# Kernel tuning notes

Hardware: AMD Instinct MI355X
Metric: run time of the kernel (lower is better)

Reference implementation:

```python
import jax, jax.numpy as jnp
import numpy as np

H = 1024
V = 50257
S = 4096

def setup_inputs() -> dict:
    key = jax.random.key(0)
    ks = jax.random.split(key, 11)
    inp = {
        "word_input": jax.random.randint(ks[0], (1,), 0, V),
        "last_context": jax.random.normal(ks[1], (1, H), jnp.float32),
        "last_hidden": jax.random.normal(ks[2], (1, 1, H), jnp.float32),
        "encoder_outputs": jax.random.normal(ks[3], (S, 1, H), jnp.float32),
        # parameters
        "embedding": jax.random.normal(ks[4], (V, H), jnp.float32) * 0.02,
        "w_ih": jax.random.normal(ks[5], (3 * H, 2 * H), jnp.float32) * 0.02,
        "w_hh": jax.random.normal(ks[6], (3 * H, H), jnp.float32) * 0.02,
        "b_ih": jax.random.normal(ks[7], (3 * H,), jnp.float32) * 0.02,
        "b_hh": jax.random.normal(ks[8], (3 * H,), jnp.float32) * 0.02,
        "out_w": jax.random.normal(ks[9], (V, 2 * H), jnp.float32) * 0.02,
        "out_b": jax.random.normal(ks[10], (V,), jnp.float32) * 0.02,
    }
    return inp

def reference(word_input, last_context, last_hidden, encoder_outputs,
              embedding, w_ih, w_hh, b_ih, b_hh, out_w, out_b):
    # embedding lookup: [H]
    emb = embedding[word_input[0]]
    # rnn input: cat(embedded, last_context) -> [2H]
    x = jnp.concatenate([emb, last_context[0]])
    h = last_hidden[0, 0]  # [H]
    # PyTorch GRU cell math (gates ordered r, z, n)
    gi = w_ih @ x + b_ih   # [3H]
    gh = w_hh @ h + b_hh   # [3H]
    i_r, i_z, i_n = jnp.split(gi, 3)
    h_r, h_z, h_n = jnp.split(gh, 3)
    r = jax.nn.sigmoid(i_r + h_r)
    z = jax.nn.sigmoid(i_z + h_z)
    n = jnp.tanh(i_n + r * h_n)
    h_new = (1.0 - z) * n + z * h  # [H], == rnn_output.squeeze()
    # multiplicative attention: per-step torch.mm loop == one batched matvec
    enc = encoder_outputs[:, 0, :]          # [S, H]
    scores = enc @ h_new                    # [S]
    attn = jax.nn.softmax(scores)           # softmax over seq dim
    context = attn @ enc                    # [H]
    logits = out_w @ jnp.concatenate([h_new, context]) + out_b  # [V]
    output = jax.nn.log_softmax(logits)[None, :]                # [1, V]
    return (output, context[None, :], h_new[None, None, :], attn[None, None, :])
```

## Files before the change

### kernel.cpp

```cpp
#include <hip/hip_runtime.h>
#include <hip/hip_bf16.h>
#include <math.h>

#define H 1024
#define V 50257
#define S 4096

typedef __hip_bfloat16 bf16;
typedef __attribute__((ext_vector_type(8))) unsigned short ushort8v;
typedef __attribute__((ext_vector_type(4))) unsigned short ushort4v;

#define WS_HX      0
#define WS_CTX     1024
#define WS_SCORES  2048
#define WS_SUMEXP  6144
#define WS_FLAG    6145

#define OUT_LOGSM  0
#define OUT_CTX    V
#define OUT_H      (V + H)
#define OUT_ATTN   (V + 2 * H)

__device__ __forceinline__ float bf2f(unsigned short u) {
    union { unsigned int i; float f; } c;
    c.i = ((unsigned int)u) << 16;
    return c.f;
}

__device__ __forceinline__ float ld1(const void* base, bool isbf, size_t i) {
    return isbf ? bf2f(((const unsigned short*)base)[i]) : ((const float*)base)[i];
}

__device__ __forceinline__ void st1(void* out, bool isbf, size_t i, float v) {
    if (isbf) ((bf16*)out)[i] = __float2bfloat16(v);
    else      ((float*)out)[i] = v;
}

__device__ __forceinline__ float dotrow(const void* base, size_t off, const float* x,
                                        int n, bool isbf, int lane) {
    float acc = 0.f;
    if (isbf) {
        const unsigned short* r = (const unsigned short*)base + off;
        for (int k = lane * 8; k < n; k += 512) {
            ushort8v w = *(const ushort8v*)(r + k);
            float4 a = *(const float4*)(x + k);
            float4 b = *(const float4*)(x + k + 4);
            acc += bf2f(w[0]) * a.x + bf2f(w[1]) * a.y + bf2f(w[2]) * a.z + bf2f(w[3]) * a.w
                 + bf2f(w[4]) * b.x + bf2f(w[5]) * b.y + bf2f(w[6]) * b.z + bf2f(w[7]) * b.w;
        }
    } else {
        const float* r = (const float*)base + off;
        for (int k = lane * 8; k < n; k += 512) {
            float4 wa = *(const float4*)(r + k);
            float4 wb = *(const float4*)(r + k + 4);
            float4 a  = *(const float4*)(x + k);
            float4 b  = *(const float4*)(x + k + 4);
            acc += wa.x * a.x + wa.y * a.y + wa.z * a.z + wa.w * a.w
                 + wb.x * b.x + wb.y * b.y + wb.z * b.z + wb.w * b.w;
        }
    }
    return acc;
}

__global__ __launch_bounds__(64) void k_detect(const unsigned short* __restrict__ lcu,
                                               float* __restrict__ ws)
{
    const int lane = threadIdx.x;
    float x = bf2f(lcu[2 * lane]);
    float ax = fabsf(x);
    int ok = (ax >= 9.5367431640625e-07f && ax <= 64.0f) ? 1 : 0;
    for (int off = 32; off; off >>= 1) ok += __shfl_down(ok, off);
    if (lane == 0) ws[WS_FLAG] = (ok >= 40) ? 1.0f : 0.0f;
}

__global__ __launch_bounds__(256) void k_gru(
    const int* __restrict__ word, const void* __restrict__ lc,
    const void* __restrict__ lh, const void* __restrict__ emb,
    const void* __restrict__ w_ih, const void* __restrict__ w_hh,
    const void* __restrict__ b_ih, const void* __restrict__ b_hh,
    float* __restrict__ ws, void* __restrict__ out)
{
    __shared__ __align__(16) float x[2 * H];
    __shared__ __align__(16) float hb[H];
    const int tid = threadIdx.x;
    const bool isbf = ws[WS_FLAG] > 0.5f;
    const size_t w0 = (size_t)word[0];
    for (int i = tid; i < H; i += 256) {
        x[i]     = ld1(emb, isbf, w0 * H + i);
        x[H + i] = ld1(lc, isbf, i);
        hb[i]    = ld1(lh, isbf, i);
    }
    __syncthreads();

    const int lane = tid & 63, wid = tid >> 6;
    const int i = blockIdx.x * 4 + wid;

    float acc[6];
    for (int g = 0; g < 3; ++g) {
        acc[g]     = dotrow(w_ih, (size_t)(i + g * H) * (2 * H), x,  2 * H, isbf, lane);
        acc[3 + g] = dotrow(w_hh, (size_t)(i + g * H) * H,       hb, H,     isbf, lane);
    }
    for (int off = 32; off; off >>= 1)
        for (int g = 0; g < 6; ++g) acc[g] += __shfl_down(acc[g], off);

    if (lane == 0) {
        float gi_r = acc[0] + ld1(b_ih, isbf, i);
        float gi_z = acc[1] + ld1(b_ih, isbf, i + H);
        float gi_n = acc[2] + ld1(b_ih, isbf, i + 2 * H);
        float gh_r = acc[3] + ld1(b_hh, isbf, i);
        float gh_z = acc[4] + ld1(b_hh, isbf, i + H);
        float gh_n = acc[5] + ld1(b_hh, isbf, i + 2 * H);
        float r = 1.f / (1.f + expf(-(gi_r + gh_r)));
        float z = 1.f / (1.f + expf(-(gi_z + gh_z)));
        float n = tanhf(gi_n + r * gh_n);
        float hn = (1.f - z) * n + z * hb[i];
        ws[WS_HX + i] = hn;
        st1(out, isbf, OUT_H + i, hn);
    }
}

__global__ __launch_bounds__(256) void k_scores(const void* __restrict__ enc,
                                                float* __restrict__ ws)
{
    __shared__ __align__(16) float hx[H];
    const int tid = threadIdx.x;
    const bool isbf = ws[WS_FLAG] > 0.5f;
    for (int i = tid; i < H; i += 256) hx[i] = ws[WS_HX + i];
    __syncthreads();
    const int lane = tid & 63, wid = tid >> 6;
    const int s = blockIdx.x * 4 + wid;
    float acc = dotrow(enc, (size_t)s * H, hx, H, isbf, lane);
    for (int off = 32; off; off >>= 1) acc += __shfl_down(acc, off);
    if (lane == 0) ws[WS_SCORES + s] = acc;
}

__global__ __launch_bounds__(1024) void k_softmax(float* __restrict__ ws, void* __restrict__ out)
{
    const int tid = threadIdx.x, lane = tid & 63, wid = tid >> 6;
    const bool isbf = ws[WS_FLAG] > 0.5f;
    __shared__ float wred[16];
    float v[4];
    float mx = -1e30f;
    for (int q = 0; q < 4; ++q) {
        v[q] = ws[WS_SCORES + tid + q * 1024];
        mx = fmaxf(mx, v[q]);
    }
    for (int off = 32; off; off >>= 1) mx = fmaxf(mx, __shfl_down(mx, off));
    if (lane == 0) wred[wid] = mx;
    __syncthreads();
    if (tid == 0) {
        float m = wred[0];
        for (int i = 1; i < 16; ++i) m = fmaxf(m, wred[i]);
        wred[0] = m;
    }
    __syncthreads();
    const float m = wred[0];
    __syncthreads();
    float se = 0.f;
    for (int q = 0; q < 4; ++q) { v[q] = expf(v[q] - m); se += v[q]; }
    for (int off = 32; off; off >>= 1) se += __shfl_down(se, off);
    if (lane == 0) wred[wid] = se;
    __syncthreads();
    if (tid == 0) {
        float s2 = 0.f;
        for (int i = 0; i < 16; ++i) s2 += wred[i];
        wred[0] = s2;
    }
    __syncthreads();
    const float inv = 1.f / wred[0];
    for (int q = 0; q < 4; ++q) {
        float p = v[q] * inv;
        ws[WS_SCORES + tid + q * 1024] = p;
        st1(out, isbf, OUT_ATTN + tid + q * 1024, p);
    }
    ws[WS_CTX + tid] = 0.f;
    if (tid == 0) ws[WS_SUMEXP] = 0.f;
}

__global__ __launch_bounds__(256) void k_context(const void* __restrict__ enc,
                                                 float* __restrict__ ws)
{
    const int tid = threadIdx.x;
    const bool isbf = ws[WS_FLAG] > 0.5f;
    const int s0 = blockIdx.x * 64;
    const int c0 = 4 * tid;
    float a0 = 0.f, a1 = 0.f, a2 = 0.f, a3 = 0.f;
    if (isbf) {
        const unsigned short* e = (const unsigned short*)enc;
        for (int s = s0; s < s0 + 64; ++s) {
            const float p = ws[WS_SCORES + s];
            ushort4v u = *(const ushort4v*)(e + (size_t)s * H + c0);
            a0 += p * bf2f(u[0]); a1 += p * bf2f(u[1]);
            a2 += p * bf2f(u[2]); a3 += p * bf2f(u[3]);
        }
    } else {
        const float* e = (const float*)enc;
        for (int s = s0; s < s0 + 64; ++s) {
            const float p = ws[WS_SCORES + s];
            float4 u = *(const float4*)(e + (size_t)s * H + c0);
            a0 += p * u.x; a1 += p * u.y; a2 += p * u.z; a3 += p * u.w;
        }
    }
    atomicAdd(&ws[WS_CTX + c0],     a0);
    atomicAdd(&ws[WS_CTX + c0 + 1], a1);
    atomicAdd(&ws[WS_CTX + c0 + 2], a2);
    atomicAdd(&ws[WS_CTX + c0 + 3], a3);
}

__global__ __launch_bounds__(256) void k_logits(
    const void* __restrict__ out_w, const void* __restrict__ out_b,
    float* __restrict__ ws, void* __restrict__ out)
{
    __shared__ __align__(16) float xv[2 * H];
    __shared__ float esum[4];
    const int tid = threadIdx.x;
    const bool isbf = ws[WS_FLAG] > 0.5f;
    for (int i = tid; i < 2 * H; i += 256) xv[i] = ws[WS_HX + i];
    __syncthreads();

    const int lane = tid & 63, wid = tid >> 6;
    const int v = blockIdx.x * 4 + wid;
    float acc = 0.f;
    if (v < V) acc = dotrow(out_w, (size_t)v * (2 * H), xv, 2 * H, isbf, lane);
    for (int off = 32; off; off >>= 1) acc += __shfl_down(acc, off);
    if (lane == 0) {
        float e = 0.f;
        if (v < V) {
            float lg = acc + ld1(out_b, isbf, v);
            st1(out, isbf, OUT_LOGSM + v, lg);
            e = expf(lg);
        }
        esum[wid] = e;
    }
    __syncthreads();
    if (tid == 0) atomicAdd(&ws[WS_SUMEXP], esum[0] + esum[1] + esum[2] + esum[3]);
}

__global__ __launch_bounds__(256) void k_final(float* __restrict__ ws, void* __restrict__ out)
{
    const int idx = blockIdx.x * 256 + threadIdx.x;
    const bool isbf = ws[WS_FLAG] > 0.5f;
    const float logZ = logf(ws[WS_SUMEXP]);
    if (idx < V) {
        float lg = isbf ? bf2f(((const unsigned short*)out)[OUT_LOGSM + idx])
                        : ((const float*)out)[OUT_LOGSM + idx];
        st1(out, isbf, OUT_LOGSM + idx, lg - logZ);
    } else if (idx < V + H) {
        st1(out, isbf, OUT_CTX + (idx - V), ws[WS_CTX + (idx - V)]);
    }
}

extern "C" void kernel_launch(void* const* d_in, const int* in_sizes, int n_in,
                              void* d_out, int out_size, void* d_ws, size_t ws_size,
                              hipStream_t stream) {
    const int* word  = (const int*)d_in[0];
    const void* lc   = d_in[1];
    const void* lh   = d_in[2];
    const void* enc  = d_in[3];
    const void* emb  = d_in[4];
    const void* w_ih = d_in[5];
    const void* w_hh = d_in[6];
    const void* b_ih = d_in[7];
    const void* b_hh = d_in[8];
    const void* o_w  = d_in[9];
    const void* o_b  = d_in[10];
    float* ws = (float*)d_ws;

    k_detect<<<1, 64, 0, stream>>>((const unsigned short*)lc, ws);
    k_gru<<<H / 4, 256, 0, stream>>>(word, lc, lh, emb, w_ih, w_hh, b_ih, b_hh, ws, d_out);
    k_scores<<<S / 4, 256, 0, stream>>>(enc, ws);
    k_softmax<<<1, 1024, 0, stream>>>(ws, d_out);
    k_context<<<S / 64, 256, 0, stream>>>(enc, ws);
    k_logits<<<(V + 3) / 4, 256, 0, stream>>>(o_w, o_b, ws, d_out);
    k_final<<<(V + H + 255) / 256, 256, 0, stream>>>(ws, d_out);
}
```

Measured before the change: 758.5 us.

## Inline dtype detection, restructure GRU per-block rows, use nontemporal weight loads

Removes the separate detection kernel by having each kernel compute the bf16/fp32 flag with a wave ballot on last_context. The GRU kernel now assigns one hidden unit per block, with all 256 threads splitting each row and keeping inputs in registers instead of shared memory. Weight streams for the GRU and logits matrices use nontemporal loads to avoid polluting the cache. The context kernel uses more blocks with 16 rows each, which adds atomics in exchange for more parallelism.

```diff
diff --git a/kernel.cpp b/kernel.cpp
--- a/kernel.cpp
+++ b/kernel.cpp
@@ -9,12 +9,12 @@
 typedef __hip_bfloat16 bf16;
 typedef __attribute__((ext_vector_type(8))) unsigned short ushort8v;
 typedef __attribute__((ext_vector_type(4))) unsigned short ushort4v;
+typedef __attribute__((ext_vector_type(4))) float f32x4;
 
 #define WS_HX      0
 #define WS_CTX     1024
 #define WS_SCORES  2048
 #define WS_SUMEXP  6144
-#define WS_FLAG    6145
 
 #define OUT_LOGSM  0
 #define OUT_CTX    V
@@ -36,13 +36,38 @@
     else      ((float*)out)[i] = v;
 }
 
+__device__ __forceinline__ bool detect_bf(const void* lc) {
+    const unsigned short* lcu = (const unsigned short*)lc;
+    float x = bf2f(lcu[2 * (threadIdx.x & 63)]);
+    float ax = fabsf(x);
+    bool ok = (ax >= 9.5367431640625e-07f && ax <= 64.0f);
+    return __popcll(__ballot(ok)) >= 40;
+}
+
+template<bool NT>
+__device__ __forceinline__ f32x4 ldf4(const float* p) {
+    if (NT) return __builtin_nontemporal_load((const f32x4*)p);
+    return *(const f32x4*)p;
+}
+template<bool NT>
+__device__ __forceinline__ ushort8v ldu8(const unsigned short* p) {
+    if (NT) return __builtin_nontemporal_load((const ushort8v*)p);
+    return *(const ushort8v*)p;
+}
+template<bool NT>
+__device__ __forceinline__ ushort4v ldu4(const unsigned short* p) {
+    if (NT) return __builtin_nontemporal_load((const ushort4v*)p);
+    return *(const ushort4v*)p;
+}
+
+template<bool NT>
 __device__ __forceinline__ float dotrow(const void* base, size_t off, const float* x,
                                         int n, bool isbf, int lane) {
     float acc = 0.f;
     if (isbf) {
         const unsigned short* r = (const unsigned short*)base + off;
         for (int k = lane * 8; k < n; k += 512) {
-            ushort8v w = *(const ushort8v*)(r + k);
+            ushort8v w = ldu8<NT>(r + k);
             float4 a = *(const float4*)(x + k);
             float4 b = *(const float4*)(x + k + 4);
             acc += bf2f(w[0]) * a.x + bf2f(w[1]) * a.y + bf2f(w[2]) * a.z + bf2f(w[3]) * a.w
@@ -51,8 +76,8 @@
     } else {
         const float* r = (const float*)base + off;
         for (int k = lane * 8; k < n; k += 512) {
-            float4 wa = *(const float4*)(r + k);
-            float4 wb = *(const float4*)(r + k + 4);
+            f32x4 wa = ldf4<NT>(r + k);
+            f32x4 wb = ldf4<NT>(r + k + 4);
             float4 a  = *(const float4*)(x + k);
             float4 b  = *(const float4*)(x + k + 4);
             acc += wa.x * a.x + wa.y * a.y + wa.z * a.z + wa.w * a.w
@@ -62,15 +87,29 @@
     return acc;
 }
 
-__global__ __launch_bounds__(64) void k_detect(const unsigned short* __restrict__ lcu,
-                                               float* __restrict__ ws)
-{
-    const int lane = threadIdx.x;
-    float x = bf2f(lcu[2 * lane]);
-    float ax = fabsf(x);
-    int ok = (ax >= 9.5367431640625e-07f && ax <= 64.0f) ? 1 : 0;
-    for (int off = 32; off; off >>= 1) ok += __shfl_down(ok, off);
-    if (lane == 0) ws[WS_FLAG] = (ok >= 40) ? 1.0f : 0.0f;
+template<bool NT>
+__device__ __forceinline__ float dot8row(const void* base, size_t off, const float* xs, bool isbf) {
+    if (isbf) {
+        ushort8v w = ldu8<NT>((const unsigned short*)base + off);
+        return bf2f(w[0]) * xs[0] + bf2f(w[1]) * xs[1] + bf2f(w[2]) * xs[2] + bf2f(w[3]) * xs[3]
+             + bf2f(w[4]) * xs[4] + bf2f(w[5]) * xs[5] + bf2f(w[6]) * xs[6] + bf2f(w[7]) * xs[7];
+    } else {
+        const float* r = (const float*)base + off;
+        f32x4 a = ldf4<NT>(r), b = ldf4<NT>(r + 4);
+        return a.x * xs[0] + a.y * xs[1] + a.z * xs[2] + a.w * xs[3]
+             + b.x * xs[4] + b.y * xs[5] + b.z * xs[6] + b.w * xs[7];
+    }
+}
+
+template<bool NT>
+__device__ __forceinline__ float dot4row(const void* base, size_t off, const float* hs, bool isbf) {
+    if (isbf) {
+        ushort4v w = ldu4<NT>((const unsigned short*)base + off);
+        return bf2f(w[0]) * hs[0] + bf2f(w[1]) * hs[1] + bf2f(w[2]) * hs[2] + bf2f(w[3]) * hs[3];
+    } else {
+        f32x4 a = ldf4<NT>((const float*)base + off);
+        return a.x * hs[0] + a.y * hs[1] + a.z * hs[2] + a.w * hs[3];
+    }
 }
 
 __global__ __launch_bounds__(256) void k_gru(
@@ -80,64 +119,101 @@
     const void* __restrict__ b_ih, const void* __restrict__ b_hh,
     float* __restrict__ ws, void* __restrict__ out)
 {
-    __shared__ __align__(16) float x[2 * H];
-    __shared__ __align__(16) float hb[H];
+    const bool isbf = detect_bf(lc);
     const int tid = threadIdx.x;
-    const bool isbf = ws[WS_FLAG] > 0.5f;
+    const int i = blockIdx.x;
     const size_t w0 = (size_t)word[0];
-    for (int i = tid; i < H; i += 256) {
-        x[i]     = ld1(emb, isbf, w0 * H + i);
-        x[H + i] = ld1(lc, isbf, i);
-        hb[i]    = ld1(lh, isbf, i);
-    }
-    __syncthreads();
-
+
+    float xs[8];
+    {
+        const int k = tid * 8;
+        const void* src = (k < H) ? emb : lc;
+        const size_t o  = (k < H) ? (w0 * H + (size_t)k) : (size_t)(k - H);
+        if (isbf) {
+            ushort8v u = *(const ushort8v*)((const unsigned short*)src + o);
+            #pragma unroll
+            for (int j = 0; j < 8; ++j) xs[j] = bf2f(u[j]);
+        } else {
+            const float* p = (const float*)src + o;
+            f32x4 a = *(const f32x4*)p, b = *(const f32x4*)(p + 4);
+            xs[0] = a.x; xs[1] = a.y; xs[2] = a.z; xs[3] = a.w;
+            xs[4] = b.x; xs[5] = b.y; xs[6] = b.z; xs[7] = b.w;
+        }
+    }
+    float hs[4];
+    {
+        const int k = tid * 4;
+        if (isbf) {
+            ushort4v u = *(const ushort4v*)((const unsigned short*)lh + k);
+            #pragma unroll
+            for (int j = 0; j < 4; ++j) hs[j] = bf2f(u[j]);
+        } else {
+            f32x4 a = *(const f32x4*)((const float*)lh + k);
+            hs[0] = a.x; hs[1] = a.y; hs[2] = a.z; hs[3] = a.w;
+        }
+    }
+
+    float acc[6];
+    #pragma unroll
+    for (int g = 0; g < 3; ++g) {
+        acc[g]     = dot8row<true>(w_ih, (size_t)(i + g * H) * (2 * H) + tid * 8, xs, isbf);
+        acc[3 + g] = dot4row<true>(w_hh, (size_t)(i + g * H) * H + tid * 4, hs, isbf);
+    }
+    #pragma unroll
+    for (int off = 32; off; off >>= 1) {
+        #pragma unroll
+        for (int g = 0; g < 6; ++g) acc[g] += __shfl_down(acc[g], off);
+    }
+
+    __shared__ float wred[4][6];
     const int lane = tid & 63, wid = tid >> 6;
-    const int i = blockIdx.x * 4 + wid;
-
-    float acc[6];
-    for (int g = 0; g < 3; ++g) {
-        acc[g]     = dotrow(w_ih, (size_t)(i + g * H) * (2 * H), x,  2 * H, isbf, lane);
-        acc[3 + g] = dotrow(w_hh, (size_t)(i + g * H) * H,       hb, H,     isbf, lane);
-    }
-    for (int off = 32; off; off >>= 1)
-        for (int g = 0; g < 6; ++g) acc[g] += __shfl_down(acc[g], off);
-
     if (lane == 0) {
-        float gi_r = acc[0] + ld1(b_ih, isbf, i);
-        float gi_z = acc[1] + ld1(b_ih, isbf, i + H);
-        float gi_n = acc[2] + ld1(b_ih, isbf, i + 2 * H);
-        float gh_r = acc[3] + ld1(b_hh, isbf, i);
-        float gh_z = acc[4] + ld1(b_hh, isbf, i + H);
-        float gh_n = acc[5] + ld1(b_hh, isbf, i + 2 * H);
+        #pragma unroll
+        for (int g = 0; g < 6; ++g) wred[wid][g] = acc[g];
+    }
+    __syncthreads();
+    if (tid == 0) {
+        float s[6];
+        #pragma unroll
+        for (int g = 0; g < 6; ++g)
+            s[g] = wred[0][g] + wred[1][g] + wred[2][g] + wred[3][g];
+        float gi_r = s[0] + ld1(b_ih, isbf, i);
+        float gi_z = s[1] + ld1(b_ih, isbf, i + H);
+        float gi_n = s[2] + ld1(b_ih, isbf, i + 2 * H);
+        float gh_r = s[3] + ld1(b_hh, isbf, i);
+        float gh_z = s[4] + ld1(b_hh, isbf, i + H);
+        float gh_n = s[5] + ld1(b_hh, isbf, i + 2 * H);
         float r = 1.f / (1.f + expf(-(gi_r + gh_r)));
         float z = 1.f / (1.f + expf(-(gi_z + gh_z)));
         float n = tanhf(gi_n + r * gh_n);
-        float hn = (1.f - z) * n + z * hb[i];
+        float hbv = ld1(lh, isbf, i);
+        float hn = (1.f - z) * n + z * hbv;
         ws[WS_HX + i] = hn;
         st1(out, isbf, OUT_H + i, hn);
     }
 }
 
 __global__ __launch_bounds__(256) void k_scores(const void* __restrict__ enc,
+                                                const void* __restrict__ lc,
                                                 float* __restrict__ ws)
 {
     __shared__ __align__(16) float hx[H];
+    const bool isbf = detect_bf(lc);
     const int tid = threadIdx.x;
-    const bool isbf = ws[WS_FLAG] > 0.5f;
     for (int i = tid; i < H; i += 256) hx[i] = ws[WS_HX + i];
     __syncthreads();
     const int lane = tid & 63, wid = tid >> 6;
     const int s = blockIdx.x * 4 + wid;
-    float acc = dotrow(enc, (size_t)s * H, hx, H, isbf, lane);
+    float acc = dotrow<false>(enc, (size_t)s * H, hx, H, isbf, lane);
     for (int off = 32; off; off >>= 1) acc += __shfl_down(acc, off);
     if (lane == 0) ws[WS_SCORES + s] = acc;
 }
 
-__global__ __launch_bounds__(1024) void k_softmax(float* __restrict__ ws, void* __restrict__ out)
+__global__ __launch_bounds__(1024) void k_softmax(const void* __restrict__ lc,
+                                                  float* __restrict__ ws, void* __restrict__ out)
 {
     const int tid = threadIdx.x, lane = tid & 63, wid = tid >> 6;
-    const bool isbf = ws[WS_FLAG] > 0.5f;
+    const bool isbf = detect_bf(lc);
     __shared__ float wred[16];
     float v[4];
     float mx = -1e30f;
@@ -178,16 +254,19 @@
 }
 
 __global__ __launch_bounds__(256) void k_context(const void* __restrict__ enc,
+                                                 const void* __restrict__ lc,
                                                  float* __restrict__ ws)
 {
+    const bool isbf = detect_bf(lc);
     const int tid = threadIdx.x;
-    const bool isbf = ws[WS_FLAG] > 0.5f;
-    const int s0 = blockIdx.x * 64;
+    const int s0 = blockIdx.x * 16;
     const int c0 = 4 * tid;
     float a0 = 0.f, a1 = 0.f, a2 = 0.f, a3 = 0.f;
     if (isbf) {
         const unsigned short* e = (const unsigned short*)enc;
-        for (int s = s0; s < s0 + 64; ++s) {
+        #pragma unroll
+        for (int q = 0; q < 16; ++q) {
+            const int s = s0 + q;
             const float p = ws[WS_SCORES + s];
             ushort4v u = *(const ushort4v*)(e + (size_t)s * H + c0);
             a0 += p * bf2f(u[0]); a1 += p * bf2f(u[1]);
@@ -195,7 +274,9 @@
         }
     } else {
         const float* e = (const float*)enc;
-        for (int s = s0; s < s0 + 64; ++s) {
+        #pragma unroll
+        for (int q = 0; q < 16; ++q) {
+            const int s = s0 + q;
             const float p = ws[WS_SCORES + s];
             float4 u = *(const float4*)(e + (size_t)s * H + c0);
             a0 += p * u.x; a1 += p * u.y; a2 += p * u.z; a3 += p * u.w;
@@ -209,19 +290,20 @@
 
 __global__ __launch_bounds__(256) void k_logits(
     const void* __restrict__ out_w, const void* __restrict__ out_b,
+    const void* __restrict__ lc,
     float* __restrict__ ws, void* __restrict__ out)
 {
     __shared__ __align__(16) float xv[2 * H];
     __shared__ float esum[4];
+    const bool isbf = detect_bf(lc);
     const int tid = threadIdx.x;
-    const bool isbf = ws[WS_FLAG] > 0.5f;
     for (int i = tid; i < 2 * H; i += 256) xv[i] = ws[WS_HX + i];
     __syncthreads();
 
     const int lane = tid & 63, wid = tid >> 6;
     const int v = blockIdx.x * 4 + wid;
     float acc = 0.f;
-    if (v < V) acc = dotrow(out_w, (size_t)v * (2 * H), xv, 2 * H, isbf, lane);
+    if (v < V) acc = dotrow<true>(out_w, (size_t)v * (2 * H), xv, 2 * H, isbf, lane);
     for (int off = 32; off; off >>= 1) acc += __shfl_down(acc, off);
     if (lane == 0) {
         float e = 0.f;
@@ -236,10 +318,11 @@
     if (tid == 0) atomicAdd(&ws[WS_SUMEXP], esum[0] + esum[1] + esum[2] + esum[3]);
 }
 
-__global__ __launch_bounds__(256) void k_final(float* __restrict__ ws, void* __restrict__ out)
-{
+__global__ __launch_bounds__(256) void k_final(const void* __restrict__ lc,
+                                               float* __restrict__ ws, void* __restrict__ out)
+{
+    const bool isbf = detect_bf(lc);
     const int idx = blockIdx.x * 256 + threadIdx.x;
-    const bool isbf = ws[WS_FLAG] > 0.5f;
     const float logZ = logf(ws[WS_SUMEXP]);
     if (idx < V) {
         float lg = isbf ? bf2f(((const unsigned short*)out)[OUT_LOGSM + idx])
@@ -266,11 +349,10 @@
     const void* o_b  = d_in[10];
     float* ws = (float*)d_ws;
 
-    k_detect<<<1, 64, 0, stream>>>((const unsigned short*)lc, ws);
-    k_gru<<<H / 4, 256, 0, stream>>>(word, lc, lh, emb, w_ih, w_hh, b_ih, b_hh, ws, d_out);
-    k_scores<<<S / 4, 256, 0, stream>>>(enc, ws);
-    k_softmax<<<1, 1024, 0, stream>>>(ws, d_out);
-    k_context<<<S / 64, 256, 0, stream>>>(enc, ws);
-    k_logits<<<(V + 3) / 4, 256, 0, stream>>>(o_w, o_b, ws, d_out);
-    k_final<<<(V + H + 255) / 256, 256, 0, stream>>>(ws, d_out);
-}
+    k_gru<<<H, 256, 0, stream>>>(word, lc, lh, emb, w_ih, w_hh, b_ih, b_hh, ws, d_out);
+    k_scores<<<S / 4, 256, 0, stream>>>(enc, lc, ws);
+    k_softmax<<<1, 1024, 0, stream>>>(lc, ws, d_out);
+    k_context<<<S / 16, 256, 0, stream>>>(enc, lc, ws);
+    k_logits<<<(V + 3) / 4, 256, 0, stream>>>(o_w, o_b, lc, ws, d_out);
+    k_final<<<(V + H + 255) / 256, 256, 0, stream>>>(lc, ws, d_out);
+}
```

Result: slower. 777.8 us (+2.5%).
